# Performance work log

Measured on AMD Instinct MI355X. Metric: run time of the kernel, lower is better.

The kernel has to match this reference:

```python
import jax, jax.numpy as jnp
import numpy as np


def _cdist_p2(x, y):
    # x: [B, N, D], y: [B, M, D] -> [B, N, M] euclidean distances
    x2 = jnp.sum(x * x, axis=-1, keepdims=True)          # [B, N, 1]
    y2 = jnp.sum(y * y, axis=-1, keepdims=True)          # [B, M, 1]
    xy = jnp.einsum('bnd,bmd->bnm', x, y)                # [B, N, M]
    d2 = x2 + jnp.swapaxes(y2, -1, -2) - 2.0 * xy
    return jnp.sqrt(jnp.maximum(d2, 0.0))


def setup_inputs() -> dict:
    key = jax.random.key(0)
    kx, ky = jax.random.split(key)
    B, N, M, D = 8, 8192, 8192, 64
    x = jax.random.normal(kx, (B, N, D), dtype=jnp.float32)
    y = jax.random.normal(ky, (B, M, D), dtype=jnp.float32)
    return {"x": x, "y": y}


def reference(x, y):
    # relative_distances: [B, N, M]
    rd = _cdist_p2(x, y)
    M = rd.shape[-1]
    a = jnp.min(rd, axis=-1)            # [B, N] nearest y for each x
    b = jnp.min(rd, axis=-2)            # [B, M] nearest x for each y
    loss_per_batch = jnp.sum(a, axis=-1) + jnp.sum(b, axis=-1)  # [B]
    return jnp.mean(loss_per_batch) / M
```

## Files before the change

### kernel.cpp

```cpp
#include <hip/hip_runtime.h>
#include <cstdint>
#include <cstddef>

typedef unsigned short u16;
typedef __attribute__((ext_vector_type(8))) short short8;
typedef __attribute__((ext_vector_type(8))) u16 ushort8;
typedef __attribute__((ext_vector_type(4))) float float4_t;

#define BB 8
#define NN 8192
#define DD 64
#define TILE_SHORTS 8192
#define LDS_STRIDE 68

__device__ inline u16 f32_to_bf16(float f) {
  unsigned u = __float_as_uint(f);
  u += 0x7FFFu + ((u >> 16) & 1u);
  return (u16)(u >> 16);
}

__device__ inline unsigned enc_ord(float f) {
  unsigned u = __float_as_uint(f);
  return (u & 0x80000000u) ? ~u : (u | 0x80000000u);
}
__device__ inline float dec_ord(unsigned u) {
  return __uint_as_float((u & 0x80000000u) ? (u & 0x7fffffffu) : ~u);
}

__global__ __launch_bounds__(256) void pre_kernel(
    const float* __restrict__ x, const float* __restrict__ y,
    u16* __restrict__ xs, u16* __restrict__ ys,
    float* __restrict__ x2h, float* __restrict__ y2h,
    unsigned* __restrict__ rowmax_u, unsigned* __restrict__ colmax_u,
    float* __restrict__ out, const int use_part)
{
  __shared__ float stage[128 * LDS_STRIDE];

  const int bid = blockIdx.x;
  const int tid = threadIdx.x;

  if (bid >= 256 && bid < 512) rowmax_u[((bid - 256) << 8) | tid] = 0u;
  if (!use_part && bid < 256)  colmax_u[(bid << 8) | tid] = 0u;
  if (bid == 0 && tid == 0) out[0] = 0.f;

  const bool isY = bid >= 512;
  const int t = bid & 511;
  const float* src = (isY ? y : x) + (size_t)t * (128 * DD);
  u16* dst = (isY ? ys : xs) + (size_t)t * TILE_SHORTS;
  float* s2 = (isY ? y2h : x2h) + t * 128;

#pragma unroll
  for (int c = 0; c < 8; ++c) {
    const int idx = c * 256 + tid;
    float4 f = ((const float4*)src)[idx];
    const int r = idx >> 4, kc = idx & 15;
    *(float4*)&stage[r * LDS_STRIDE + kc * 4] = f;
  }
  __syncthreads();

  {
    const int r = tid >> 1, half = tid & 1;
    const float* rp = &stage[r * LDS_STRIDE + half * 32];
    float ss = 0.f;
#pragma unroll
    for (int k = 0; k < 8; ++k) {
      float4 f = *(const float4*)&rp[k * 4];
      ss += f.x*f.x + f.y*f.y + f.z*f.z + f.w*f.w;
    }
    ss += __shfl_xor(ss, 1);
    if (half == 0) s2[r] = 0.5f * ss;
  }

  {
    const int w = tid >> 6, lane = tid & 63;
    const int qq = lane >> 4, rl = lane & 15;
#pragma unroll
    for (int u = 0; u < 4; ++u) {
      const int chunk = w * 4 + u;
      const int I = chunk >> 1, s = chunk & 1;
      const float* rp = &stage[(I*16 + rl) * LDS_STRIDE + s*32 + qq*8];
      ushort8 o;
#pragma unroll
      for (int j = 0; j < 8; ++j) o[j] = f32_to_bf16(rp[j]);
      *(ushort8*)(dst + chunk*512 + lane*8) = o;
    }
  }
}

__global__ __launch_bounds__(256, 3) void main_kernel(
    const u16* __restrict__ xs, const u16* __restrict__ ys,
    const float* __restrict__ x2h, const float* __restrict__ y2h,
    float* __restrict__ colpart,
    unsigned* __restrict__ rowmax_u, unsigned* __restrict__ colmax_u,
    const int use_part)
{
  __shared__ unsigned colbufu[2048];
  __shared__ float rowbuf[2][128];

  const int bid = blockIdx.x;
  const int b   = bid & 7;
  const int nt  = (bid >> 3) & 63;
  const int h   = bid >> 9;
  const int tid = threadIdx.x;
  const int w = tid >> 6, lane = tid & 63;
  const int wr = w >> 1, wc = w & 1;
  const int l15 = lane & 15, q = lane >> 4;
  const int n0 = nt << 7;
  const int mt_start = h << 4;

#pragma unroll
  for (int k = 0; k < 8; ++k) colbufu[k * 256 + tid] = 0u;

  const u16* xs_tile = xs + (size_t)((b << 6) | nt) * TILE_SHORTS;
  short8 afr[4][2];
#pragma unroll
  for (int i = 0; i < 4; ++i)
#pragma unroll
    for (int s = 0; s < 2; ++s)
      afr[i][s] = *(const short8*)(xs_tile + ((wr*4 + i)*2 + s)*512 + lane*8);

  float4_t negx2[4];
  const float* x2b = x2h + b*NN + n0 + wr*64;
#pragma unroll
  for (int i = 0; i < 4; ++i) {
    float4_t v = *(const float4_t*)(x2b + i*16 + q*4);
    negx2[i] = {-v[0], -v[1], -v[2], -v[3]};
  }

  float rowmax[4][4];
#pragma unroll
  for (int i = 0; i < 4; ++i)
#pragma unroll
    for (int r = 0; r < 4; ++r) rowmax[i][r] = -3.0e38f;

  const u16*  pB = ys + (size_t)((b << 6) + mt_start) * TILE_SHORTS
                   + wc*4096 + lane*8;
  const float* pY = y2h + b*NN + mt_start*128 + wc*64 + l15;

  short8 b0lo, b0hi, b1lo, b1hi, b2lo, b2hi, b3lo, b3hi;
  float  y20, y21, y22, y23;
  b0lo = *(const short8*)(pB);
  b0hi = *(const short8*)(pB + 512);
  y20  = pY[0];
  b1lo = *(const short8*)(pB + 1024);
  b1hi = *(const short8*)(pB + 1536);
  y21  = pY[16];
  y23  = 0.f;

  float4_t accA[4], accB[4];
#pragma unroll
  for (int i = 0; i < 4; ++i)
    accB[i] = {-3.0e38f, -3.0e38f, -3.0e38f, -3.0e38f};

  __syncthreads();

  int moff = 0;
  for (int mt = 0; mt < 16; ++mt) {
    const int mprev = (moff == 0) ? 0 : (moff - 128);
#define CHAM_STEP(JJ, NOFF, NY, C0, C1, YC, N0, N1, YN, AC, AP, PJJ, PYC, PMOFF) \
    {                                                                         \
      N0 = *(const short8*)(pB + (NOFF));                                     \
      N1 = *(const short8*)(pB + (NOFF) + 512);                               \
      YN = pY[(NY)];                                                          \
                            \
      __builtin_amdgcn_s_setprio(1);                                          \
      AC[0] = __builtin_amdgcn_mfma_f32_16x16x32_bf16(afr[0][0], C0, negx2[0], 0, 0, 0); \
      AC[1] = __builtin_amdgcn_mfma_f32_16x16x32_bf16(afr[1][0], C0, negx2[1], 0, 0, 0); \
      AC[2] = __builtin_amdgcn_mfma_f32_16x16x32_bf16(afr[2][0], C0, negx2[2], 0, 0, 0); \
      AC[3] = __builtin_amdgcn_mfma_f32_16x16x32_bf16(afr[3][0], C0, negx2[3], 0, 0, 0); \
      AC[0] = __builtin_amdgcn_mfma_f32_16x16x32_bf16(afr[0][1], C1, AC[0], 0, 0, 0);    \
      AC[1] = __builtin_amdgcn_mfma_f32_16x16x32_bf16(afr[1][1], C1, AC[1], 0, 0, 0);    \
      AC[2] = __builtin_amdgcn_mfma_f32_16x16x32_bf16(afr[2][1], C1, AC[2], 0, 0, 0);    \
      AC[3] = __builtin_amdgcn_mfma_f32_16x16x32_bf16(afr[3][1], C1, AC[3], 0, 0, 0);    \
      __builtin_amdgcn_s_setprio(0);                                          \
       \
       \
      float t0 = fmaxf(fmaxf(AP[0][0], AP[0][1]), AP[0][2]);                  \
      float t1 = fmaxf(fmaxf(AP[0][3], AP[1][0]), AP[1][1]);                  \
      float t2 = fmaxf(fmaxf(AP[1][2], AP[1][3]), AP[2][0]);                  \
      float t3 = fmaxf(fmaxf(AP[2][1], AP[2][2]), AP[2][3]);                  \
      float t4 = fmaxf(fmaxf(AP[3][0], AP[3][1]), AP[3][2]);                  \
      float u0 = fmaxf(fmaxf(t0, t1), t2);                                    \
      float u1 = fmaxf(fmaxf(t3, t4), AP[3][3]);                              \
      float cm = fmaxf(u0, u1);                                               \
      atomicMax(&colbufu[(PMOFF) + wc*64 + (PJJ)*16 + l15], enc_ord(cm));     \
                         \
      {                                                                       \
        const float y2j = (PYC);                                              \
        for (int i_ = 0; i_ < 4; ++i_)                                        \
          for (int r_ = 0; r_ < 4; ++r_)                                      \
            rowmax[i_][r_] = fmaxf(rowmax[i_][r_], AP[i_][r_] - y2j);         \
      }                                                                       \
    }
    CHAM_STEP(0, 2048,              32,  b0lo, b0hi, y20, b2lo, b2hi, y22,
              accA, accB, 3, y23, mprev)
    CHAM_STEP(1, 3072,              48,  b1lo, b1hi, y21, b3lo, b3hi, y23,
              accB, accA, 0, y20, moff)
    CHAM_STEP(2, TILE_SHORTS,       128, b2lo, b2hi, y22, b0lo, b0hi, y20,
              accA, accB, 1, y21, moff)
    CHAM_STEP(3, TILE_SHORTS+1024,  144, b3lo, b3hi, y23, b1lo, b1hi, y21,
              accB, accA, 2, y22, moff)
#undef CHAM_STEP
    pB += TILE_SHORTS;
    pY += 128;
    moff += 128;
  }

  {
    const int pmoff = moff - 128;
    float t0 = fmaxf(fmaxf(accB[0][0], accB[0][1]), accB[0][2]);
    float t1 = fmaxf(fmaxf(accB[0][3], accB[1][0]), accB[1][1]);
    float t2 = fmaxf(fmaxf(accB[1][2], accB[1][3]), accB[2][0]);
    float t3 = fmaxf(fmaxf(accB[2][1], accB[2][2]), accB[2][3]);
    float t4 = fmaxf(fmaxf(accB[3][0], accB[3][1]), accB[3][2]);
    float u0 = fmaxf(fmaxf(t0, t1), t2);
    float u1 = fmaxf(fmaxf(t3, t4), accB[3][3]);
    float cm = fmaxf(u0, u1);
    atomicMax(&colbufu[pmoff + wc*64 + 3*16 + l15], enc_ord(cm));
    const float y2j = y23;
#pragma unroll
    for (int i_ = 0; i_ < 4; ++i_)
#pragma unroll
      for (int r_ = 0; r_ < 4; ++r_)
        rowmax[i_][r_] = fmaxf(rowmax[i_][r_], accB[i_][r_] - y2j);
  }

#pragma unroll
  for (int i = 0; i < 4; ++i)
#pragma unroll
    for (int r = 0; r < 4; ++r) {
      float v = rowmax[i][r];
      v = fmaxf(v, __shfl_xor(v, 1));
      v = fmaxf(v, __shfl_xor(v, 2));
      v = fmaxf(v, __shfl_xor(v, 4));
      v = fmaxf(v, __shfl_xor(v, 8));
      rowmax[i][r] = v;
    }
  if (l15 == 0) {
#pragma unroll
    for (int i = 0; i < 4; ++i)
#pragma unroll
      for (int r = 0; r < 4; ++r)
        rowbuf[wc][wr*64 + i*16 + q*4 + r] = rowmax[i][r];
  }
  __syncthreads();

  if (tid < 128) {
    float v = fmaxf(rowbuf[0][tid], rowbuf[1][tid]);
    atomicMax(&rowmax_u[b*NN + n0 + tid], enc_ord(v));
  }

  {
    float*    colp = colpart + (size_t)((b << 6) | nt) * NN + (h << 11);
    unsigned* colu = colmax_u + b*NN + (h << 11);
#pragma unroll
    for (int k = 0; k < 8; ++k) {
      const int t = k * 256 + tid;
      const unsigned e = colbufu[t];
      if (use_part) colp[t] = dec_ord(e);
      else          atomicMax(&colu[t], e);
    }
  }
}

__global__ __launch_bounds__(256) void reduce_kernel(
    const float* __restrict__ colpart,
    const unsigned* __restrict__ rowmax_u, const unsigned* __restrict__ colmax_u,
    const float* __restrict__ y2h, float* __restrict__ out,
    const int use_part)
{
  const int bid = blockIdx.x;
  const int tid = threadIdx.x;
  const int g = bid*256 + tid;
  const int b = g >> 13, m = g & (NN - 1);

  float vc;
  if (use_part) {
    vc = -3.0e38f;
#pragma unroll 8
    for (int nt = 0; nt < 64; ++nt)
      vc = fmaxf(vc, colpart[(size_t)((b << 6) | nt) * NN + m]);
  } else {
    vc = dec_ord(colmax_u[g]);
  }
  float vr = dec_ord(rowmax_u[g]);
  float s = sqrtf(fmaxf(2.f*(y2h[g] - vc), 0.f))
          + sqrtf(fmaxf(-2.f*vr, 0.f));

#pragma unroll
  for (int d = 1; d < 64; d <<= 1) s += __shfl_xor(s, d);
  __shared__ float wsum[4];
  if ((tid & 63) == 0) wsum[tid >> 6] = s;
  __syncthreads();
  if (tid == 0)
    atomicAdd(out, (wsum[0] + wsum[1] + wsum[2] + wsum[3]) * (1.0f / 65536.0f));
}

extern "C" void kernel_launch(void* const* d_in, const int* in_sizes, int n_in,
                              void* d_out, int out_size, void* d_ws, size_t ws_size,
                              hipStream_t stream) {
  const float* x = (const float*)d_in[0];
  const float* y = (const float*)d_in[1];
  float* out = (float*)d_out;

  char* p = (char*)d_ws;
  u16* xs = (u16*)p;            p += (size_t)512 * 16384;
  u16* ys = (u16*)p;            p += (size_t)512 * 16384;
  float* x2h = (float*)p;       p += (size_t)65536 * 4;
  float* y2h = (float*)p;       p += (size_t)65536 * 4;
  char* tail = p;
  float* colpart = (float*)tail;
  unsigned* colmax_u = (unsigned*)tail;
  const size_t need_part = (size_t)(tail - (char*)d_ws) +
                           (size_t)512 * 8192 * 4 + (size_t)65536 * 4;
  const int use_part = (ws_size >= need_part) ? 1 : 0;
  unsigned* rowmax_u = use_part
      ? (unsigned*)(tail + (size_t)512 * 8192 * 4)
      : (unsigned*)(tail + (size_t)65536 * 4);

  pre_kernel<<<dim3(1024), dim3(256), 0, stream>>>(x, y, xs, ys, x2h, y2h,
                                                   rowmax_u, colmax_u, out,
                                                   use_part);
  main_kernel<<<dim3(2048), dim3(256), 0, stream>>>(xs, ys, x2h, y2h,
                                                    colpart,
                                                    rowmax_u, colmax_u,
                                                    use_part);
  reduce_kernel<<<dim3(256), dim3(256), 0, stream>>>(colpart,
                                                     rowmax_u, colmax_u, y2h,
                                                     out, use_part);
}
```

Baseline: 158.7 us.

## Split main kernel across 8 waves with 32 rows per wave

The main kernel now launches 512 threads per block, and each wave covers 32 x-rows instead of 64. The per-wave A fragments, accumulators and rowmax registers are halved, so more waves can be resident to hide latency. The cost is that each wave now streams the same B tiles for half as many MFMAs, doubling B global/L2 load traffic per compute and adding more LDS atomics for the column maxima. The pre-kernel also reads the staged LDS values as float4 vectors instead of scalars.

```diff
diff --git a/kernel.cpp b/kernel.cpp
--- a/kernel.cpp
+++ b/kernel.cpp
@@ -79,15 +79,19 @@
       const int chunk = w * 4 + u;
       const int I = chunk >> 1, s = chunk & 1;
       const float* rp = &stage[(I*16 + rl) * LDS_STRIDE + s*32 + qq*8];
+      float4 f0 = *(const float4*)&rp[0];
+      float4 f1 = *(const float4*)&rp[4];
       ushort8 o;
-#pragma unroll
-      for (int j = 0; j < 8; ++j) o[j] = f32_to_bf16(rp[j]);
+      o[0] = f32_to_bf16(f0.x); o[1] = f32_to_bf16(f0.y);
+      o[2] = f32_to_bf16(f0.z); o[3] = f32_to_bf16(f0.w);
+      o[4] = f32_to_bf16(f1.x); o[5] = f32_to_bf16(f1.y);
+      o[6] = f32_to_bf16(f1.z); o[7] = f32_to_bf16(f1.w);
       *(ushort8*)(dst + chunk*512 + lane*8) = o;
     }
   }
 }
 
-__global__ __launch_bounds__(256, 3) void main_kernel(
+__global__ __launch_bounds__(512, 4) void main_kernel(
     const u16* __restrict__ xs, const u16* __restrict__ ys,
     const float* __restrict__ x2h, const float* __restrict__ y2h,
     float* __restrict__ colpart,
@@ -103,33 +107,33 @@
   const int h   = bid >> 9;
   const int tid = threadIdx.x;
   const int w = tid >> 6, lane = tid & 63;
-  const int wr = w >> 1, wc = w & 1;
+  const int rq = w >> 1, wc = w & 1;
   const int l15 = lane & 15, q = lane >> 4;
   const int n0 = nt << 7;
   const int mt_start = h << 4;
 
 #pragma unroll
-  for (int k = 0; k < 8; ++k) colbufu[k * 256 + tid] = 0u;
+  for (int k = 0; k < 4; ++k) colbufu[k * 512 + tid] = 0u;
 
   const u16* xs_tile = xs + (size_t)((b << 6) | nt) * TILE_SHORTS;
-  short8 afr[4][2];
-#pragma unroll
-  for (int i = 0; i < 4; ++i)
+  short8 afr[2][2];
+#pragma unroll
+  for (int i = 0; i < 2; ++i)
 #pragma unroll
     for (int s = 0; s < 2; ++s)
-      afr[i][s] = *(const short8*)(xs_tile + ((wr*4 + i)*2 + s)*512 + lane*8);
-
-  float4_t negx2[4];
-  const float* x2b = x2h + b*NN + n0 + wr*64;
-#pragma unroll
-  for (int i = 0; i < 4; ++i) {
+      afr[i][s] = *(const short8*)(xs_tile + ((rq*2 + i)*2 + s)*512 + lane*8);
+
+  float4_t negx2[2];
+  const float* x2b = x2h + b*NN + n0 + rq*32;
+#pragma unroll
+  for (int i = 0; i < 2; ++i) {
     float4_t v = *(const float4_t*)(x2b + i*16 + q*4);
     negx2[i] = {-v[0], -v[1], -v[2], -v[3]};
   }
 
-  float rowmax[4][4];
-#pragma unroll
-  for (int i = 0; i < 4; ++i)
+  float rowmax[2][4];
+#pragma unroll
+  for (int i = 0; i < 2; ++i)
 #pragma unroll
     for (int r = 0; r < 4; ++r) rowmax[i][r] = -3.0e38f;
 
@@ -147,9 +151,9 @@
   y21  = pY[16];
   y23  = 0.f;
 
-  float4_t accA[4], accB[4];
-#pragma unroll
-  for (int i = 0; i < 4; ++i)
+  float4_t accA[2], accB[2];
+#pragma unroll
+  for (int i = 0; i < 2; ++i)
     accB[i] = {-3.0e38f, -3.0e38f, -3.0e38f, -3.0e38f};
 
   __syncthreads();
@@ -166,28 +170,20 @@
       __builtin_amdgcn_s_setprio(1);                                          \
       AC[0] = __builtin_amdgcn_mfma_f32_16x16x32_bf16(afr[0][0], C0, negx2[0], 0, 0, 0); \
       AC[1] = __builtin_amdgcn_mfma_f32_16x16x32_bf16(afr[1][0], C0, negx2[1], 0, 0, 0); \
-      AC[2] = __builtin_amdgcn_mfma_f32_16x16x32_bf16(afr[2][0], C0, negx2[2], 0, 0, 0); \
-      AC[3] = __builtin_amdgcn_mfma_f32_16x16x32_bf16(afr[3][0], C0, negx2[3], 0, 0, 0); \
       AC[0] = __builtin_amdgcn_mfma_f32_16x16x32_bf16(afr[0][1], C1, AC[0], 0, 0, 0);    \
       AC[1] = __builtin_amdgcn_mfma_f32_16x16x32_bf16(afr[1][1], C1, AC[1], 0, 0, 0);    \
-      AC[2] = __builtin_amdgcn_mfma_f32_16x16x32_bf16(afr[2][1], C1, AC[2], 0, 0, 0);    \
-      AC[3] = __builtin_amdgcn_mfma_f32_16x16x32_bf16(afr[3][1], C1, AC[3], 0, 0, 0);    \
       __builtin_amdgcn_s_setprio(0);                                          \
        \
        \
-      float t0 = fmaxf(fmaxf(AP[0][0], AP[0][1]), AP[0][2]);                  \
-      float t1 = fmaxf(fmaxf(AP[0][3], AP[1][0]), AP[1][1]);                  \
-      float t2 = fmaxf(fmaxf(AP[1][2], AP[1][3]), AP[2][0]);                  \
-      float t3 = fmaxf(fmaxf(AP[2][1], AP[2][2]), AP[2][3]);                  \
-      float t4 = fmaxf(fmaxf(AP[3][0], AP[3][1]), AP[3][2]);                  \
-      float u0 = fmaxf(fmaxf(t0, t1), t2);                                    \
-      float u1 = fmaxf(fmaxf(t3, t4), AP[3][3]);                              \
-      float cm = fmaxf(u0, u1);                                               \
+      float m1 = fmaxf(fmaxf(AP[0][0], AP[0][1]), AP[0][2]);                  \
+      float m2 = fmaxf(fmaxf(AP[0][3], AP[1][0]), AP[1][1]);                  \
+      float m3 = fmaxf(AP[1][2], AP[1][3]);                                   \
+      float cm = fmaxf(fmaxf(m1, m2), m3);                                    \
       atomicMax(&colbufu[(PMOFF) + wc*64 + (PJJ)*16 + l15], enc_ord(cm));     \
                          \
       {                                                                       \
         const float y2j = (PYC);                                              \
-        for (int i_ = 0; i_ < 4; ++i_)                                        \
+        for (int i_ = 0; i_ < 2; ++i_)                                        \
           for (int r_ = 0; r_ < 4; ++r_)                                      \
             rowmax[i_][r_] = fmaxf(rowmax[i_][r_], AP[i_][r_] - y2j);         \
       }                                                                       \
@@ -208,25 +204,21 @@
 
   {
     const int pmoff = moff - 128;
-    float t0 = fmaxf(fmaxf(accB[0][0], accB[0][1]), accB[0][2]);
-    float t1 = fmaxf(fmaxf(accB[0][3], accB[1][0]), accB[1][1]);
-    float t2 = fmaxf(fmaxf(accB[1][2], accB[1][3]), accB[2][0]);
-    float t3 = fmaxf(fmaxf(accB[2][1], accB[2][2]), accB[2][3]);
-    float t4 = fmaxf(fmaxf(accB[3][0], accB[3][1]), accB[3][2]);
-    float u0 = fmaxf(fmaxf(t0, t1), t2);
-    float u1 = fmaxf(fmaxf(t3, t4), accB[3][3]);
-    float cm = fmaxf(u0, u1);
+    float m1 = fmaxf(fmaxf(accB[0][0], accB[0][1]), accB[0][2]);
+    float m2 = fmaxf(fmaxf(accB[0][3], accB[1][0]), accB[1][1]);
+    float m3 = fmaxf(accB[1][2], accB[1][3]);
+    float cm = fmaxf(fmaxf(m1, m2), m3);
     atomicMax(&colbufu[pmoff + wc*64 + 3*16 + l15], enc_ord(cm));
     const float y2j = y23;
 #pragma unroll
-    for (int i_ = 0; i_ < 4; ++i_)
+    for (int i_ = 0; i_ < 2; ++i_)
 #pragma unroll
       for (int r_ = 0; r_ < 4; ++r_)
         rowmax[i_][r_] = fmaxf(rowmax[i_][r_], accB[i_][r_] - y2j);
   }
 
 #pragma unroll
-  for (int i = 0; i < 4; ++i)
+  for (int i = 0; i < 2; ++i)
 #pragma unroll
     for (int r = 0; r < 4; ++r) {
       float v = rowmax[i][r];
@@ -238,10 +230,10 @@
     }
   if (l15 == 0) {
 #pragma unroll
-    for (int i = 0; i < 4; ++i)
+    for (int i = 0; i < 2; ++i)
 #pragma unroll
       for (int r = 0; r < 4; ++r)
-        rowbuf[wc][wr*64 + i*16 + q*4 + r] = rowmax[i][r];
+        rowbuf[wc][rq*32 + i*16 + q*4 + r] = rowmax[i][r];
   }
   __syncthreads();
 
@@ -254,8 +246,8 @@
     float*    colp = colpart + (size_t)((b << 6) | nt) * NN + (h << 11);
     unsigned* colu = colmax_u + b*NN + (h << 11);
 #pragma unroll
-    for (int k = 0; k < 8; ++k) {
-      const int t = k * 256 + tid;
+    for (int k = 0; k < 4; ++k) {
+      const int t = k * 512 + tid;
       const unsigned e = colbufu[t];
       if (use_part) colp[t] = dec_ord(e);
       else          atomicMax(&colu[t], e);
@@ -321,7 +313,7 @@
   pre_kernel<<<dim3(1024), dim3(256), 0, stream>>>(x, y, xs, ys, x2h, y2h,
                                                    rowmax_u, colmax_u, out,
                                                    use_part);
-  main_kernel<<<dim3(2048), dim3(256), 0, stream>>>(xs, ys, x2h, y2h,
+  main_kernel<<<dim3(2048), dim3(512), 0, stream>>>(xs, ys, x2h, y2h,
                                                     colpart,
                                                     rowmax_u, colmax_u,
                                                     use_part);
```

Result: slower. 178.5 us (+12.5%).
